# Optimization experiments

Measured on AMD Instinct MI355X. Metric: run time of the kernel, lower is better.

## Reference

```python
import jax, jax.numpy as jnp
import numpy as np

# Fixed hierarchical grouping of the 15 regions into 5 groups of 3 (from split_regions)
SPLIT_IDX = np.array([[0, 1, 8], [2, 4, 6], [3, 5, 7], [9, 11, 13], [10, 12, 14]])
BN_EPS = 1e-5


def _bn_relu(x, g, b):
    # BatchNorm over (batch, spatial) dims in training-stats mode, then ReLU
    mu = jnp.mean(x, axis=(0, 2, 3), keepdims=True)
    var = jnp.var(x, axis=(0, 2, 3), keepdims=True)
    xn = (x - mu) * jax.lax.rsqrt(var + BN_EPS)
    return jax.nn.relu(xn * g[None, :, None, None] + b[None, :, None, None])


def _local_agg(x, params):
    # x: [B, Cin, G, K]; pointwise conv (1x1) -> BN -> ReLU per layer, then max over K
    for W, g, b in params:
        x = jnp.einsum('oi,bigk->bogk', W, x)
        x = _bn_relu(x, g, b)
    return jnp.max(x, axis=-1)  # [B, Cout, G]


def setup_inputs() -> dict:
    key = jax.random.key(0)
    ks = jax.random.split(key, 8)
    B, G, K = 32, 15, 2048
    inp = {"local_regions": jax.random.normal(ks[0], (B, G, K, 3), jnp.float32)}
    chans = [(3, 64, 64), (67, 128, 128), (131, 256, 256)]
    ki = 1
    for li, (c0, c1, c2) in enumerate(chans):
        for wi, (co, ci) in enumerate([(c1, c0), (c2, c1)]):
            inp[f"la{li}_w{wi}"] = jax.random.normal(ks[ki], (co, ci), jnp.float32) * (1.0 / np.sqrt(ci))
            inp[f"la{li}_g{wi}"] = jnp.ones((co,), jnp.float32)
            inp[f"la{li}_b{wi}"] = jnp.zeros((co,), jnp.float32)
            ki += 1
    return inp


def reference(local_regions,
              la0_w0, la0_g0, la0_b0, la0_w1, la0_g1, la0_b1,
              la1_w0, la1_g0, la1_b0, la1_w1, la1_g1, la1_b1,
              la2_w0, la2_g0, la2_b0, la2_w1, la2_g1, la2_b1):
    la0 = [(la0_w0, la0_g0, la0_b0), (la0_w1, la0_g1, la0_b1)]
    la1 = [(la1_w0, la1_g0, la1_b0), (la1_w1, la1_g1, la1_b1)]
    la2 = [(la2_w0, la2_g0, la2_b0), (la2_w1, la2_g1, la2_b1)]
    idx = jnp.asarray(SPLIT_IDX)

    x = jnp.transpose(local_regions, (0, 3, 1, 2))  # [B, 3, 15, K]
    centroids_1 = jnp.mean(x, axis=-1)              # [B, 3, 15]
    relative_1 = x - centroids_1[..., None]
    lf1 = _local_agg(relative_1, la0)               # [B, 64, 15]
    local_features = jnp.concatenate([centroids_1, lf1], axis=1)  # [B, 67, 15]

    # level 2: regroup 15 regions into [5, 3]
    lf1_s = jnp.transpose(lf1, (0, 2, 1))[:, idx, :]         # [B, 5, 3, 64]
    lr2 = jnp.transpose(centroids_1, (0, 2, 1))[:, idx, :]   # [B, 5, 3, 3]
    c2 = jnp.mean(lr2, axis=2)                               # [B, 5, 3]
    rel2 = lr2 - c2[:, :, None, :]
    feats2 = jnp.concatenate([rel2, lf1_s], axis=-1)         # [B, 5, 3, 67]
    feats2 = jnp.transpose(feats2, (0, 3, 1, 2))             # [B, 67, 5, 3]
    lf2 = _local_agg(feats2, la1)                            # [B, 128, 5]

    # level 3: global
    c3 = jnp.mean(c2, axis=1)                                # [B, 3]
    rel3 = c2 - c3[:, None, :]                               # [B, 5, 3]
    lf2 = jnp.concatenate([jnp.transpose(rel3, (0, 2, 1)), lf2], axis=1)  # [B, 131, 5]
    lf2 = lf2[:, :, None, :]                                 # [B, 131, 1, 5]
    gf = _local_agg(lf2, la2)                                # [B, 256, 1]
    return gf.squeeze(2), local_features
```

## Files before the change

kernel.cpp:

```cpp
#include <hip/hip_runtime.h>
#include <math.h>

#define BB 32
#define GG 15
#define KK 2048
#define NB 480
#define N1F 983040.0f
#define EPS 1e-5f
#define PZN ((int)0xAAAAAAAA)

typedef _Float16 half8 __attribute__((ext_vector_type(8)));
typedef float f32x4 __attribute__((ext_vector_type(4)));

#define WS_CENT  0
#define WS_MN    1920
#define GSREL    63360
#define GBN1     63600
#define G2A      67440
#define G2B      67952
#define G3A      68464
#define G3B      69488
#define FSREL    70512
#define FBN1     70520
#define F2A      70648
#define F2B      70904
#define F3A      71160
#define F3B      71672
#define CNT_GRP  72184
#define CNT_SUP  72376
#define CNT_DONE 72382

#define SMEMF 7936

__device__ const int SIDX[15] = {0,1,8, 2,4,6, 3,5,7, 9,11,13, 10,12,14};

__device__ __forceinline__ float wave_sum(float v){
    for (int off = 32; off; off >>= 1) v += __shfl_down(v, off, 64);
    return v;
}
__device__ __forceinline__ float aloadf(const float* p){
    return __hip_atomic_load(p, __ATOMIC_RELAXED, __HIP_MEMORY_SCOPE_AGENT);
}
__device__ __forceinline__ int aloadi(const int* p){
    return __hip_atomic_load(p, __ATOMIC_RELAXED, __HIP_MEMORY_SCOPE_AGENT);
}
template<int SLP, class Fold>
__device__ __forceinline__ void gbar(int* wsi, int idx, int gi, int ngrp,
                                     int* sflag, Fold fold){
    __syncthreads();
    if (threadIdx.x == 0)
        sflag[0] = (atomicAdd(&wsi[CNT_GRP + idx*32 + gi], 1) == PZN + 15) ? 1 : 0;
    __syncthreads();
    if (sflag[0]) {
        if (threadIdx.x == 0)
            sflag[1] = (atomicAdd(&wsi[CNT_SUP + idx], 1) == PZN + ngrp - 1) ? 1 : 0;
        __syncthreads();
        if (sflag[1]) {
            fold();
            __syncthreads();
            if (threadIdx.x == 0) atomicExch(&wsi[CNT_DONE + idx], 1);
        }
    }
    if (threadIdx.x == 0) {
        int g = 0;
        while (aloadi(&wsi[CNT_DONE + idx]) != 1 && ++g < 4000000)
            __builtin_amdgcn_s_sleep(SLP);
    }
    __syncthreads();
    asm volatile("" ::: "memory");
}

__global__ void __launch_bounds__(256, 2) mega(
        const float* __restrict__ x,
        const float* __restrict__ w00, const float* __restrict__ g00, const float* __restrict__ b00,
        const float* __restrict__ w01, const float* __restrict__ g01, const float* __restrict__ b01,
        const float* __restrict__ w10, const float* __restrict__ g10, const float* __restrict__ b10,
        const float* __restrict__ w11, const float* __restrict__ g11, const float* __restrict__ b11,
        const float* __restrict__ w20, const float* __restrict__ g20, const float* __restrict__ b20,
        const float* __restrict__ w21, const float* __restrict__ g21, const float* __restrict__ b21,
        float* __restrict__ ws, float* __restrict__ out) {
    __shared__ __align__(16) float smemf[SMEMF];
    float* xls  = smemf;
    float* redM = smemf + 6144; float* redN = smemf + 6400;
    float* redS = smemf + 6656; float* redQ = smemf + 6912;
    float* bcast= smemf + 7168;
    int*   sflag= (int*)(smemf + 7916);
    float* s1ls  = smemf;
    float* t1ls  = smemf + 64;
    float* centls= smemf + 128;
    float* c2ls  = smemf + 176;
    float* c3ls  = smemf + 192;
    float* f2ls  = smemf + 256;
    float* vls   = smemf + 1280;
    float* f3ls  = smemf + 3200;
    float* u3ls  = smemf + 3968;
    int* wsi = (int*)ws;

    int bid = blockIdx.x, tid = threadIdx.x;
    int b_ = bid / GG, g_ = bid % GG;
    int wv = tid >> 6, lane = tid & 63, l15 = lane & 15, quad = lane >> 4;
    int gi = bid >> 4;

    {
        const float4* xp4 = (const float4*)(x + (size_t)bid * KK * 3);
        float4* xls4 = (float4*)xls;
        #pragma unroll
        for (int i = 0; i < 6; i++) xls4[i*256 + tid] = xp4[i*256 + tid];
        __syncthreads();
        float m[9] = {0,0,0,0,0,0,0,0,0};
        float a[24];
        const float* bp = &xls[tid*24];
        #pragma unroll
        for (int i = 0; i < 6; i++)
            *reinterpret_cast<float4*>(&a[i*4]) = *reinterpret_cast<const float4*>(&bp[i*4]);
        #pragma unroll
        for (int p = 0; p < 8; p++) {
            float ax=a[p*3], ay=a[p*3+1], az=a[p*3+2];
            m[0]+=ax; m[1]+=ay; m[2]+=az;
            m[3]=fmaf(ax,ax,m[3]); m[4]=fmaf(ay,ay,m[4]); m[5]=fmaf(az,az,m[5]);
            m[6]=fmaf(ax,ay,m[6]); m[7]=fmaf(ax,az,m[7]); m[8]=fmaf(ay,az,m[8]);
        }
        #pragma unroll
        for (int q = 0; q < 9; q++) {
            float v = wave_sum(m[q]);
            if (lane == 0) redM[q*4 + wv] = v;
        }
        __syncthreads();
        if (tid == 0) {
            float t[9];
            #pragma unroll
            for (int q = 0; q < 9; q++) t[q] = redM[q*4]+redM[q*4+1]+redM[q*4+2]+redM[q*4+3];
            float c0 = t[0]/KK, c1 = t[1]/KK, c2 = t[2]/KK;
            bcast[0]=c0; bcast[1]=c1; bcast[2]=c2;
            out[8192 + b_*(67*GG) + 0*GG + g_] = c0;
            out[8192 + b_*(67*GG) + 1*GG + g_] = c1;
            out[8192 + b_*(67*GG) + 2*GG + g_] = c2;
            atomicExch(&ws[WS_CENT + bid*4 + 0], c0);
            atomicExch(&ws[WS_CENT + bid*4 + 1], c1);
            atomicExch(&ws[WS_CENT + bid*4 + 2], c2);
            redM[40] = t[3] - KK*c0*c0;  redM[41] = t[4] - KK*c1*c1;
            redM[42] = t[5] - KK*c2*c2;  redM[43] = t[6] - KK*c0*c1;
            redM[44] = t[7] - KK*c0*c2;  redM[45] = t[8] - KK*c1*c2;
        }
        __syncthreads();
    }
    if (tid < 6) atomicAdd(&ws[GSREL + gi*8 + tid], redM[40 + tid]);

    half8 afA[4], afB[4];
    #pragma unroll
    for (int t = 0; t < 4; t++)
        #pragma unroll
        for (int j = 0; j < 8; j++) {
            afA[t][j] = (_Float16)w01[(t*16 + l15)*64 + quad*8 + j];
            afB[t][j] = (_Float16)w01[(t*16 + l15)*64 + 32 + quad*8 + j];
        }
    gbar<8>(wsi, 0, gi, 30, sflag, [&]{
        if (tid < 6) {
            float acc = 0.f;
            #pragma unroll
            for (int s = 0; s < 30; s++) acc += aloadf(&ws[GSREL + s*8 + tid]);
            atomicExch(&ws[FSREL + tid], acc);
        }
    });

    if (tid < 6) bcast[3+tid] = aloadf(&ws[FSREL + tid]) / N1F;
    __syncthreads();
    float c0 = bcast[0], c1 = bcast[1], c2v = bcast[2];
    float S00=bcast[3], S11=bcast[4], S22=bcast[5], S01=bcast[6], S02=bcast[7], S12=bcast[8];

    float wa0[8], wa1[8], wa2[8], ba[8], wb0[8], wb1[8], wb2[8], bb[8];
    #pragma unroll
    for (int j = 0; j < 8; j++) {
        int cA = quad*8 + j;
        float u0=w00[cA*3+0], u1=w00[cA*3+1], u2=w00[cA*3+2];
        float var = u0*u0*S00 + u1*u1*S11 + u2*u2*S22
                  + 2.f*(u0*u1*S01 + u0*u2*S02 + u1*u2*S12);
        float a1 = g00[cA]*rsqrtf(var + EPS);
        wa0[j]=a1*u0; wa1[j]=a1*u1; wa2[j]=a1*u2; ba[j]=b00[cA];
        int cB = cA + 32;
        float v0=w00[cB*3+0], v1=w00[cB*3+1], v2=w00[cB*3+2];
        float varB = v0*v0*S00 + v1*v1*S11 + v2*v2*S22
                   + 2.f*(v0*v1*S01 + v0*v2*S02 + v1*v2*S12);
        float a1B = g00[cB]*rsqrtf(varB + EPS);
        wb0[j]=a1B*v0; wb1[j]=a1B*v1; wb2[j]=a1B*v2; bb[j]=b00[cB];
    }
    float mx[16], mn[16], sm[16], sq[16];
    #pragma unroll
    for (int s = 0; s < 16; s++) { mx[s]=-1e30f; mn[s]=1e30f; sm[s]=0.f; sq[s]=0.f; }

    for (int it = 0; it < 32; it++) {
        int k = it*64 + wv*16 + l15;
        float r0 = xls[k*3+0]-c0, r1 = xls[k*3+1]-c1, r2 = xls[k*3+2]-c2v;
        half8 bf0, bf1;
        #pragma unroll
        for (int j = 0; j < 8; j++) {
            float pA = fmaf(wa0[j],r0, fmaf(wa1[j],r1, fmaf(wa2[j],r2, ba[j])));
            bf0[j] = (_Float16)fmaxf(pA, 0.f);
            float pB = fmaf(wb0[j],r0, fmaf(wb1[j],r1, fmaf(wb2[j],r2, bb[j])));
            bf1[j] = (_Float16)fmaxf(pB, 0.f);
        }
        #pragma unroll
        for (int t = 0; t < 4; t++) {
            f32x4 acc = {0.f,0.f,0.f,0.f};
            acc = __builtin_amdgcn_mfma_f32_16x16x32_f16(afA[t], bf0, acc, 0, 0, 0);
            acc = __builtin_amdgcn_mfma_f32_16x16x32_f16(afB[t], bf1, acc, 0, 0, 0);
            #pragma unroll
            for (int r = 0; r < 4; r++) {
                float h = acc[r];
                int s = t*4 + r;
                mx[s]=fmaxf(mx[s],h); mn[s]=fminf(mn[s],h);
                sm[s]+=h;             sq[s]=fmaf(h,h,sq[s]);
            }
        }
    }
    #pragma unroll
    for (int m = 1; m < 16; m <<= 1) {
        #pragma unroll
        for (int s = 0; s < 16; s++) {
            mx[s] = fmaxf(mx[s], __shfl_xor(mx[s], m, 64));
            mn[s] = fminf(mn[s], __shfl_xor(mn[s], m, 64));
            sm[s] += __shfl_xor(sm[s], m, 64);
            sq[s] += __shfl_xor(sq[s], m, 64);
        }
    }
    __syncthreads();
    if (l15 == 0) {
        #pragma unroll
        for (int t = 0; t < 4; t++)
            #pragma unroll
            for (int r = 0; r < 4; r++) {
                int o = t*16 + quad*4 + r;
                redM[wv*64+o]=mx[t*4+r]; redN[wv*64+o]=mn[t*4+r];
                redS[wv*64+o]=sm[t*4+r]; redQ[wv*64+o]=sq[t*4+r];
            }
    }
    __syncthreads();
    float Mreg = -1e30f, Nreg = 1e30f;
    if (tid < 64) {
        float S=0.f, Q=0.f;
        #pragma unroll
        for (int w = 0; w < 4; w++) {
            Mreg = fmaxf(Mreg, redM[w*64+tid]); Nreg = fminf(Nreg, redN[w*64+tid]);
            S += redS[w*64+tid];               Q += redQ[w*64+tid];
        }
        atomicAdd(&ws[GBN1 + gi*128 + tid], S);
        atomicAdd(&ws[GBN1 + gi*128 + 64 + tid], Q);
        atomicExch(&ws[WS_MN + bid*128 + tid], Mreg);
        atomicExch(&ws[WS_MN + bid*128 + 64 + tid], Nreg);
    }
    gbar<8>(wsi, 1, gi, 30, sflag, [&]{
        if (tid < 128) {
            float acc = 0.f;
            #pragma unroll
            for (int s = 0; s < 30; s++) acc += aloadf(&ws[GBN1 + s*128 + tid]);
            atomicExch(&ws[FBN1 + tid], acc);
        }
    });

    if (tid < 64) {
        float SM = aloadf(&ws[FBN1 + tid]);
        float SQ = aloadf(&ws[FBN1 + 64 + tid]);
        float mean = SM / N1F;
        float var  = SQ / N1F - mean*mean;
        float s1 = g01[tid]*rsqrtf(var + EPS);
        float t1 = b01[tid] - mean*s1;
        float val = fmaxf(fmaf(s1, (s1 >= 0.f) ? Mreg : Nreg, t1), 0.f);
        out[8192 + b_*(67*GG) + (3+tid)*GG + g_] = val;
        s1ls[tid] = s1; t1ls[tid] = t1;
    }
    if (g_ != 0) return;

    int git = b_ >> 4;
    if (tid < 45) centls[tid] = aloadf(&ws[WS_CENT + (b_*GG + tid/3)*4 + tid%3]);
    __syncthreads();
    if (tid < 15) {
        int s = tid/3, i = tid%3;
        c2ls[tid] = (centls[SIDX[s*3+0]*3+i] + centls[SIDX[s*3+1]*3+i]
                   + centls[SIDX[s*3+2]*3+i]) * (1.f/3.f);
    }
    __syncthreads();
    if (tid < 3)
        c3ls[tid] = (c2ls[tid]+c2ls[3+tid]+c2ls[6+tid]+c2ls[9+tid]+c2ls[12+tid]) * 0.2f;
    if (tid < 45) {
        int p = tid/3, i = tid%3;
        f2ls[p*68 + i] = centls[SIDX[p]*3+i] - c2ls[(p/3)*3 + i];
    }
    for (int u = tid; u < 960; u += 256) {
        int p = u >> 6, ch = u & 63, gsrc = SIDX[p];
        float Mv = aloadf(&ws[WS_MN + (b_*GG + gsrc)*128 + ch]);
        float Nv = aloadf(&ws[WS_MN + (b_*GG + gsrc)*128 + 64 + ch]);
        float s1 = s1ls[ch], t1 = t1ls[ch];
        f2ls[p*68 + 3 + ch] = fmaxf(fmaf(s1, (s1 >= 0.f) ? Mv : Nv, t1), 0.f);
    }
    __syncthreads();

    int half = tid >> 7, oc = tid & 127, pbase = half*8, npts = 8 - half;
    float acc[8];
    #pragma unroll
    for (int q = 0; q < 8; q++) acc[q] = 0.f;
    {
        const float* wr = w10 + oc*67;
        #pragma unroll 4
        for (int c = 0; c < 67; c++) {
            float wv_ = wr[c];
            #pragma unroll
            for (int q = 0; q < 8; q++)
                acc[q] = fmaf(wv_, f2ls[(pbase+q)*68 + c], acc[q]);
        }
        float S = 0.f, Q = 0.f;
        #pragma unroll
        for (int q = 0; q < 8; q++) if (q < npts) { S += acc[q]; Q = fmaf(acc[q],acc[q],Q); }
        redS[tid] = S; redQ[tid] = Q;
        __syncthreads();
        if (tid < 128) {
            atomicAdd(&ws[G2A + git*256 + tid],       redS[tid] + redS[tid+128]);
            atomicAdd(&ws[G2A + git*256 + 128 + tid], redQ[tid] + redQ[tid+128]);
        }
    }
    gbar<2>(wsi, 2, git, 2, sflag, [&]{
        float a = aloadf(&ws[G2A + tid]) + aloadf(&ws[G2A + 256 + tid]);
        atomicExch(&ws[F2A + tid], a);
    });

    {
        float mean = aloadf(&ws[F2A + oc]) / 480.f;
        float var  = aloadf(&ws[F2A + 128 + oc]) / 480.f - mean*mean;
        float s2 = g10[oc]*rsqrtf(var + EPS), t2 = b10[oc] - mean*s2;
        #pragma unroll
        for (int q = 0; q < 8; q++) {
            float v = fmaxf(fmaf(s2, acc[q], t2), 0.f);
            if (q < npts) vls[(pbase+q)*128 + oc] = v;
        }
    }
    __syncthreads();
    #pragma unroll
    for (int q = 0; q < 8; q++) acc[q] = 0.f;
    {
        const float* wr = w11 + oc*128;
        #pragma unroll 4
        for (int c = 0; c < 128; c++) {
            float wv_ = wr[c];
            #pragma unroll
            for (int q = 0; q < 8; q++)
                acc[q] = fmaf(wv_, vls[(pbase+q)*128 + c], acc[q]);
        }
        float S = 0.f, Q = 0.f;
        #pragma unroll
        for (int q = 0; q < 8; q++) if (q < npts) { S += acc[q]; Q = fmaf(acc[q],acc[q],Q); }
        redS[tid] = S; redQ[tid] = Q;
        __syncthreads();
        if (tid < 128) {
            atomicAdd(&ws[G2B + git*256 + tid],       redS[tid] + redS[tid+128]);
            atomicAdd(&ws[G2B + git*256 + 128 + tid], redQ[tid] + redQ[tid+128]);
        }
    }
    gbar<2>(wsi, 3, git, 2, sflag, [&]{
        float a = aloadf(&ws[G2B + tid]) + aloadf(&ws[G2B + 256 + tid]);
        atomicExch(&ws[F2B + tid], a);
    });

    {
        float mean = aloadf(&ws[F2B + oc]) / 480.f;
        float var  = aloadf(&ws[F2B + 128 + oc]) / 480.f - mean*mean;
        float s3 = g11[oc]*rsqrtf(var + EPS), t3 = b11[oc] - mean*s3;
        #pragma unroll
        for (int q = 0; q < 8; q++) {
            float v = fmaxf(fmaf(s3, acc[q], t3), 0.f);
            if (q < npts) vls[(pbase+q)*128 + oc] = v;
        }
    }
    __syncthreads();
    for (int u = tid; u < 640; u += 256) {
        int s = u >> 7, o2 = u & 127;
        float m = fmaxf(fmaxf(vls[(3*s)*128+o2], vls[(3*s+1)*128+o2]),
                        vls[(3*s+2)*128+o2]);
        f3ls[s*132 + 3 + o2] = m;
    }
    if (tid < 15) {
        int s = tid/3, i = tid%3;
        f3ls[s*132 + i] = c2ls[tid] - c3ls[i];
    }
    __syncthreads();

    float a3[5];
    #pragma unroll
    for (int s = 0; s < 5; s++) a3[s] = 0.f;
    {
        const float* wr = w20 + tid*131;
        #pragma unroll 4
        for (int c = 0; c < 131; c++) {
            float wv_ = wr[c];
            #pragma unroll
            for (int s = 0; s < 5; s++)
                a3[s] = fmaf(wv_, f3ls[s*132 + c], a3[s]);
        }
        float S = 0.f, Q = 0.f;
        #pragma unroll
        for (int s = 0; s < 5; s++) { S += a3[s]; Q = fmaf(a3[s],a3[s],Q); }
        atomicAdd(&ws[G3A + git*512 + tid], S);
        atomicAdd(&ws[G3A + git*512 + 256 + tid], Q);
    }
    gbar<2>(wsi, 4, git, 2, sflag, [&]{
        float a0 = aloadf(&ws[G3A + tid])       + aloadf(&ws[G3A + 512 + tid]);
        float a1 = aloadf(&ws[G3A + 256 + tid]) + aloadf(&ws[G3A + 512 + 256 + tid]);
        atomicExch(&ws[F3A + tid], a0);
        atomicExch(&ws[F3A + 256 + tid], a1);
    });

    {
        float mean = aloadf(&ws[F3A + tid]) / 160.f;
        float var  = aloadf(&ws[F3A + 256 + tid]) / 160.f - mean*mean;
        float s4 = g20[tid]*rsqrtf(var + EPS), t4 = b20[tid] - mean*s4;
        #pragma unroll
        for (int s = 0; s < 5; s++)
            u3ls[s*256 + tid] = fmaxf(fmaf(s4, a3[s], t4), 0.f);
    }
    __syncthreads();
    #pragma unroll
    for (int s = 0; s < 5; s++) a3[s] = 0.f;
    {
        const float* wr = w21 + tid*256;
        #pragma unroll 4
        for (int c = 0; c < 256; c++) {
            float wv_ = wr[c];
            #pragma unroll
            for (int s = 0; s < 5; s++)
                a3[s] = fmaf(wv_, u3ls[s*256 + c], a3[s]);
        }
        float S = 0.f, Q = 0.f;
        #pragma unroll
        for (int s = 0; s < 5; s++) { S += a3[s]; Q = fmaf(a3[s],a3[s],Q); }
        atomicAdd(&ws[G3B + git*512 + tid], S);
        atomicAdd(&ws[G3B + git*512 + 256 + tid], Q);
    }
    gbar<2>(wsi, 5, git, 2, sflag, [&]{
        float a0 = aloadf(&ws[G3B + tid])       + aloadf(&ws[G3B + 512 + tid]);
        float a1 = aloadf(&ws[G3B + 256 + tid]) + aloadf(&ws[G3B + 512 + 256 + tid]);
        atomicExch(&ws[F3B + tid], a0);
        atomicExch(&ws[F3B + 256 + tid], a1);
    });

    {
        float mean = aloadf(&ws[F3B + tid]) / 160.f;
        float var  = aloadf(&ws[F3B + 256 + tid]) / 160.f - mean*mean;
        float s5 = g21[tid]*rsqrtf(var + EPS), t5 = b21[tid] - mean*s5;
        float m = -1e30f;
        #pragma unroll
        for (int s = 0; s < 5; s++)
            m = fmaxf(m, fmaxf(fmaf(s5, a3[s], t5), 0.f));
        out[b_*256 + tid] = m;
    }
}

extern "C" void kernel_launch(void* const* d_in, const int* in_sizes, int n_in,
                              void* d_out, int out_size, void* d_ws, size_t ws_size,
                              hipStream_t stream) {
    (void)in_sizes; (void)n_in; (void)out_size; (void)ws_size;
    const float* x   = (const float*)d_in[0];
    const float* w00 = (const float*)d_in[1];
    const float* g00 = (const float*)d_in[2];
    const float* b00 = (const float*)d_in[3];
    const float* w01 = (const float*)d_in[4];
    const float* g01 = (const float*)d_in[5];
    const float* b01 = (const float*)d_in[6];
    const float* w10 = (const float*)d_in[7];
    const float* g10 = (const float*)d_in[8];
    const float* b10 = (const float*)d_in[9];
    const float* w11 = (const float*)d_in[10];
    const float* g11 = (const float*)d_in[11];
    const float* b11 = (const float*)d_in[12];
    const float* w20 = (const float*)d_in[13];
    const float* g20 = (const float*)d_in[14];
    const float* b20 = (const float*)d_in[15];
    const float* w21 = (const float*)d_in[16];
    const float* g21 = (const float*)d_in[17];
    const float* b21 = (const float*)d_in[18];
    float* out = (float*)d_out;
    float* ws  = (float*)d_ws;

    mega<<<NB, 256, 0, stream>>>(x, w00,g00,b00, w01,g01,b01, w10,g10,b10,
                                 w11,g11,b11, w20,g20,b20, w21,g21,b21, ws, out);
}
```

Before: 191.1 us.

## Replace hierarchical fold barriers with flat counter barriers and per-batch partial slots

Measured after the change: 203.8 us. +6.6%, slower.

```diff
diff --git a/kernel.cpp b/kernel.cpp
--- a/kernel.cpp
+++ b/kernel.cpp
@@ -1,7 +1,6 @@
 #include <hip/hip_runtime.h>
 #include <math.h>
 
-#define BB 32
 #define GG 15
 #define KK 2048
 #define NB 480
@@ -12,23 +11,22 @@
 typedef _Float16 half8 __attribute__((ext_vector_type(8)));
 typedef float f32x4 __attribute__((ext_vector_type(4)));
 
-#define WS_CENT  0
-#define WS_MN    1920
-#define GSREL    63360
-#define GBN1     63600
-#define G2A      67440
-#define G2B      67952
-#define G3A      68464
-#define G3B      69488
-#define FSREL    70512
-#define FBN1     70520
-#define F2A      70648
-#define F2B      70904
-#define F3A      71160
-#define F3B      71672
-#define CNT_GRP  72184
-#define CNT_SUP  72376
-#define CNT_DONE 72382
+#define CENT  0
+#define GSREL 1920
+#define GBN1  2160
+#define SELO  6256
+#define FBN1  36976
+#define P2A   37104
+#define P2B   45296
+#define P3A   53488
+#define P3B   69872
+#define CA0   86256
+#define CA1   86272
+#define CD1   86288
+#define CT2   86304
+#define CT3   86320
+#define CT4   86336
+#define CT5   86352
 
 #define SMEMF 7936
 
@@ -44,26 +42,13 @@
 __device__ __forceinline__ int aloadi(const int* p){
     return __hip_atomic_load(p, __ATOMIC_RELAXED, __HIP_MEMORY_SCOPE_AGENT);
 }
-template<int SLP, class Fold>
-__device__ __forceinline__ void gbar(int* wsi, int idx, int gi, int ngrp,
-                                     int* sflag, Fold fold){
-    __syncthreads();
-    if (threadIdx.x == 0)
-        sflag[0] = (atomicAdd(&wsi[CNT_GRP + idx*32 + gi], 1) == PZN + 15) ? 1 : 0;
-    __syncthreads();
-    if (sflag[0]) {
-        if (threadIdx.x == 0)
-            sflag[1] = (atomicAdd(&wsi[CNT_SUP + idx], 1) == PZN + ngrp - 1) ? 1 : 0;
-        __syncthreads();
-        if (sflag[1]) {
-            fold();
-            __syncthreads();
-            if (threadIdx.x == 0) atomicExch(&wsi[CNT_DONE + idx], 1);
-        }
-    }
+template<int SLP>
+__device__ __forceinline__ void fbar(int* c, int target){
+    __syncthreads();
     if (threadIdx.x == 0) {
+        atomicAdd(c, 1);
         int g = 0;
-        while (aloadi(&wsi[CNT_DONE + idx]) != 1 && ++g < 4000000)
+        while (aloadi(c) != target && ++g < 8000000)
             __builtin_amdgcn_s_sleep(SLP);
     }
     __syncthreads();
@@ -84,16 +69,17 @@
     float* redM = smemf + 6144; float* redN = smemf + 6400;
     float* redS = smemf + 6656; float* redQ = smemf + 6912;
     float* bcast= smemf + 7168;
-    int*   sflag= (int*)(smemf + 7916);
     float* s1ls  = smemf;
     float* t1ls  = smemf + 64;
-    float* centls= smemf + 128;
-    float* c2ls  = smemf + 176;
-    float* c3ls  = smemf + 192;
-    float* f2ls  = smemf + 256;
-    float* vls   = smemf + 1280;
-    float* f3ls  = smemf + 3200;
-    float* u3ls  = smemf + 3968;
+    float* centb = smemf + 128;
+    float* c2b   = smemf + 176;
+    float* c3b   = smemf + 192;
+    float* f2b   = smemf + 256;
+    float* vb    = smemf + 1344;
+    float* f3b   = smemf + 3392;
+    float* u3b   = smemf + 4052;
+    float* c2s   = smemf + 5332;
+    float* c2t   = smemf + 5460;
     int* wsi = (int*)ws;
 
     int bid = blockIdx.x, tid = threadIdx.x;
@@ -135,9 +121,9 @@
             out[8192 + b_*(67*GG) + 0*GG + g_] = c0;
             out[8192 + b_*(67*GG) + 1*GG + g_] = c1;
             out[8192 + b_*(67*GG) + 2*GG + g_] = c2;
-            atomicExch(&ws[WS_CENT + bid*4 + 0], c0);
-            atomicExch(&ws[WS_CENT + bid*4 + 1], c1);
-            atomicExch(&ws[WS_CENT + bid*4 + 2], c2);
+            atomicExch(&ws[CENT + bid*4 + 0], c0);
+            atomicExch(&ws[CENT + bid*4 + 1], c1);
+            atomicExch(&ws[CENT + bid*4 + 2], c2);
             redM[40] = t[3] - KK*c0*c0;  redM[41] = t[4] - KK*c1*c1;
             redM[42] = t[5] - KK*c2*c2;  redM[43] = t[6] - KK*c0*c1;
             redM[44] = t[7] - KK*c0*c2;  redM[45] = t[8] - KK*c1*c2;
@@ -154,16 +140,15 @@
             afA[t][j] = (_Float16)w01[(t*16 + l15)*64 + quad*8 + j];
             afB[t][j] = (_Float16)w01[(t*16 + l15)*64 + 32 + quad*8 + j];
         }
-    gbar<8>(wsi, 0, gi, 30, sflag, [&]{
-        if (tid < 6) {
-            float acc = 0.f;
-            #pragma unroll
-            for (int s = 0; s < 30; s++) acc += aloadf(&ws[GSREL + s*8 + tid]);
-            atomicExch(&ws[FSREL + tid], acc);
-        }
-    });
-
-    if (tid < 6) bcast[3+tid] = aloadf(&ws[FSREL + tid]) / N1F;
+
+    fbar<4>(&wsi[CA0], PZN + 480);
+
+    if (tid < 6) {
+        float acc = 0.f;
+        #pragma unroll
+        for (int s = 0; s < 30; s++) acc += aloadf(&ws[GSREL + s*8 + tid]);
+        bcast[3+tid] = acc / N1F;
+    }
     __syncthreads();
     float c0 = bcast[0], c1 = bcast[1], c2v = bcast[2];
     float S00=bcast[3], S11=bcast[4], S22=bcast[5], S01=bcast[6], S02=bcast[7], S12=bcast[8];
@@ -243,25 +228,43 @@
             Mreg = fmaxf(Mreg, redM[w*64+tid]); Nreg = fminf(Nreg, redN[w*64+tid]);
             S += redS[w*64+tid];               Q += redQ[w*64+tid];
         }
-        atomicAdd(&ws[GBN1 + gi*128 + tid], S);
-        atomicAdd(&ws[GBN1 + gi*128 + 64 + tid], Q);
-        atomicExch(&ws[WS_MN + bid*128 + tid], Mreg);
-        atomicExch(&ws[WS_MN + bid*128 + 64 + tid], Nreg);
-    }
-    gbar<8>(wsi, 1, gi, 30, sflag, [&]{
+        atomicAdd(&ws[GBN1 + b_*128 + tid], S);
+        atomicAdd(&ws[GBN1 + b_*128 + 64 + tid], Q);
+        float sel = (g01[tid] >= 0.f) ? Mreg : Nreg;
+        atomicExch(&ws[SELO + bid*64 + tid], sel);
+    }
+
+    __syncthreads();
+    if (tid == 0) atomicAdd(&wsi[CA1], 1);
+    if (bid == 0) {
+        if (tid == 0) {
+            int g = 0;
+            while (aloadi(&wsi[CA1]) != PZN + 480 && ++g < 8000000)
+                __builtin_amdgcn_s_sleep(2);
+        }
+        __syncthreads();
         if (tid < 128) {
             float acc = 0.f;
             #pragma unroll
-            for (int s = 0; s < 30; s++) acc += aloadf(&ws[GBN1 + s*128 + tid]);
+            for (int i = 0; i < 32; i++) acc += aloadf(&ws[GBN1 + i*128 + tid]);
             atomicExch(&ws[FBN1 + tid], acc);
         }
-    });
+        __syncthreads();
+        if (tid == 0) atomicAdd(&wsi[CD1], 1);
+    }
+    if (tid == 0) {
+        int g = 0;
+        while (aloadi(&wsi[CD1]) != PZN + 1 && ++g < 8000000)
+            __builtin_amdgcn_s_sleep(2);
+    }
+    __syncthreads();
+    asm volatile("" ::: "memory");
 
     if (tid < 64) {
-        float SM = aloadf(&ws[FBN1 + tid]);
-        float SQ = aloadf(&ws[FBN1 + 64 + tid]);
-        float mean = SM / N1F;
-        float var  = SQ / N1F - mean*mean;
+        float S = aloadf(&ws[FBN1 + tid]);
+        float Q = aloadf(&ws[FBN1 + 64 + tid]);
+        float mean = S / N1F;
+        float var  = Q / N1F - mean*mean;
         float s1 = g01[tid]*rsqrtf(var + EPS);
         float t1 = b01[tid] - mean*s1;
         float val = fmaxf(fmaf(s1, (s1 >= 0.f) ? Mreg : Nreg, t1), 0.f);
@@ -270,184 +273,208 @@
     }
     if (g_ != 0) return;
 
-    int git = b_ >> 4;
-    if (tid < 45) centls[tid] = aloadf(&ws[WS_CENT + (b_*GG + tid/3)*4 + tid%3]);
-    __syncthreads();
-    if (tid < 15) {
-        int s = tid/3, i = tid%3;
-        c2ls[tid] = (centls[SIDX[s*3+0]*3+i] + centls[SIDX[s*3+1]*3+i]
-                   + centls[SIDX[s*3+2]*3+i]) * (1.f/3.f);
-    }
-    __syncthreads();
-    if (tid < 3)
-        c3ls[tid] = (c2ls[tid]+c2ls[3+tid]+c2ls[6+tid]+c2ls[9+tid]+c2ls[12+tid]) * 0.2f;
-    if (tid < 45) {
-        int p = tid/3, i = tid%3;
-        f2ls[p*68 + i] = centls[SIDX[p]*3+i] - c2ls[(p/3)*3 + i];
-    }
-    for (int u = tid; u < 960; u += 256) {
-        int p = u >> 6, ch = u & 63, gsrc = SIDX[p];
-        float Mv = aloadf(&ws[WS_MN + (b_*GG + gsrc)*128 + ch]);
-        float Nv = aloadf(&ws[WS_MN + (b_*GG + gsrc)*128 + 64 + ch]);
-        float s1 = s1ls[ch], t1 = t1ls[ch];
-        f2ls[p*68 + 3 + ch] = fmaxf(fmaf(s1, (s1 >= 0.f) ? Mv : Nv, t1), 0.f);
-    }
-    __syncthreads();
-
-    int half = tid >> 7, oc = tid & 127, pbase = half*8, npts = 8 - half;
-    float acc[8];
-    #pragma unroll
-    for (int q = 0; q < 8; q++) acc[q] = 0.f;
+    int half_ = tid >> 7, oc = tid & 127, pbase = half_*8, npts = 8 - half_;
+    float acc1[8], acc2[8], a3[5], a3b[5];
+
     {
+        if (tid < 45) centb[tid] = aloadf(&ws[CENT + (b_*GG + tid/3)*4 + tid%3]);
+        if (tid >= 188) f2b[15*68 + (tid - 188)] = 0.f;
+        __syncthreads();
+        if (tid < 15) {
+            int s = tid/3, i = tid%3;
+            c2b[tid] = (centb[SIDX[s*3+0]*3+i] + centb[SIDX[s*3+1]*3+i]
+                      + centb[SIDX[s*3+2]*3+i]) * (1.f/3.f);
+        }
+        __syncthreads();
+        if (tid < 3)
+            c3b[tid] = (c2b[tid]+c2b[3+tid]+c2b[6+tid]+c2b[9+tid]+c2b[12+tid]) * 0.2f;
+        if (tid < 45) {
+            int p = tid/3, i = tid%3;
+            f2b[p*68 + i] = centb[SIDX[p]*3+i] - c2b[(p/3)*3 + i];
+        }
+        for (int u = tid; u < 960; u += 256) {
+            int p = u >> 6, ch = u & 63, src = b_*GG + SIDX[p];
+            float sel = aloadf(&ws[SELO + src*64 + ch]);
+            f2b[p*68 + 3 + ch] = fmaxf(fmaf(s1ls[ch], sel, t1ls[ch]), 0.f);
+        }
+        __syncthreads();
+        #pragma unroll
+        for (int q = 0; q < 8; q++) acc1[q] = 0.f;
         const float* wr = w10 + oc*67;
         #pragma unroll 4
         for (int c = 0; c < 67; c++) {
             float wv_ = wr[c];
             #pragma unroll
             for (int q = 0; q < 8; q++)
-                acc[q] = fmaf(wv_, f2ls[(pbase+q)*68 + c], acc[q]);
+                acc1[q] = fmaf(wv_, f2b[(pbase+q)*68 + c], acc1[q]);
         }
         float S = 0.f, Q = 0.f;
         #pragma unroll
-        for (int q = 0; q < 8; q++) if (q < npts) { S += acc[q]; Q = fmaf(acc[q],acc[q],Q); }
+        for (int q = 0; q < 8; q++) if (q < npts) { S += acc1[q]; Q = fmaf(acc1[q],acc1[q],Q); }
         redS[tid] = S; redQ[tid] = Q;
         __syncthreads();
         if (tid < 128) {
-            atomicAdd(&ws[G2A + git*256 + tid],       redS[tid] + redS[tid+128]);
-            atomicAdd(&ws[G2A + git*256 + 128 + tid], redQ[tid] + redQ[tid+128]);
-        }
-    }
-    gbar<2>(wsi, 2, git, 2, sflag, [&]{
-        float a = aloadf(&ws[G2A + tid]) + aloadf(&ws[G2A + 256 + tid]);
-        atomicExch(&ws[F2A + tid], a);
-    });
+            atomicExch(&ws[P2A + b_*256 + tid],       redS[tid] + redS[128 + tid]);
+            atomicExch(&ws[P2A + b_*256 + 128 + tid], redQ[tid] + redQ[128 + tid]);
+        }
+    }
+    fbar<1>(&wsi[CT2], PZN + 32);
 
     {
-        float mean = aloadf(&ws[F2A + oc]) / 480.f;
-        float var  = aloadf(&ws[F2A + 128 + oc]) / 480.f - mean*mean;
-        float s2 = g10[oc]*rsqrtf(var + EPS), t2 = b10[oc] - mean*s2;
-        #pragma unroll
-        for (int q = 0; q < 8; q++) {
-            float v = fmaxf(fmaf(s2, acc[q], t2), 0.f);
-            if (q < npts) vls[(pbase+q)*128 + oc] = v;
-        }
-    }
-    __syncthreads();
-    #pragma unroll
-    for (int q = 0; q < 8; q++) acc[q] = 0.f;
+        if (tid < 128) {
+            float S = 0.f, Q = 0.f;
+            #pragma unroll
+            for (int i = 0; i < 32; i++) {
+                S += aloadf(&ws[P2A + i*256 + tid]);
+                Q += aloadf(&ws[P2A + i*256 + 128 + tid]);
+            }
+            float mean = S / 480.f, var = Q / 480.f - mean*mean;
+            float s2 = g10[tid]*rsqrtf(var + EPS);
+            c2s[tid] = s2; c2t[tid] = b10[tid] - mean*s2;
+            vb[15*128 + tid] = 0.f;
+        }
+        __syncthreads();
+        {
+            float s2 = c2s[oc], t2 = c2t[oc];
+            #pragma unroll
+            for (int q = 0; q < 8; q++) {
+                float v = fmaxf(fmaf(s2, acc1[q], t2), 0.f);
+                if (q < npts) vb[(pbase+q)*128 + oc] = v;
+            }
+        }
+        __syncthreads();
+        #pragma unroll
+        for (int q = 0; q < 8; q++) acc2[q] = 0.f;
+        const float4* w4 = (const float4*)(w11 + oc*128);
+        #pragma unroll 2
+        for (int c4 = 0; c4 < 32; c4++) {
+            float4 wv4 = w4[c4];
+            int cb = c4*4;
+            #pragma unroll
+            for (int q = 0; q < 8; q++) {
+                const float* vrow = &vb[(pbase+q)*128];
+                acc2[q] = fmaf(wv4.x, vrow[cb+0], acc2[q]);
+                acc2[q] = fmaf(wv4.y, vrow[cb+1], acc2[q]);
+                acc2[q] = fmaf(wv4.z, vrow[cb+2], acc2[q]);
+                acc2[q] = fmaf(wv4.w, vrow[cb+3], acc2[q]);
+            }
+        }
+        float S = 0.f, Q = 0.f;
+        #pragma unroll
+        for (int q = 0; q < 8; q++) if (q < npts) { S += acc2[q]; Q = fmaf(acc2[q],acc2[q],Q); }
+        redS[tid] = S; redQ[tid] = Q;
+        __syncthreads();
+        if (tid < 128) {
+            atomicExch(&ws[P2B + b_*256 + tid],       redS[tid] + redS[128 + tid]);
+            atomicExch(&ws[P2B + b_*256 + 128 + tid], redQ[tid] + redQ[128 + tid]);
+        }
+    }
+    fbar<1>(&wsi[CT3], PZN + 32);
+
     {
-        const float* wr = w11 + oc*128;
-        #pragma unroll 4
-        for (int c = 0; c < 128; c++) {
-            float wv_ = wr[c];
-            #pragma unroll
-            for (int q = 0; q < 8; q++)
-                acc[q] = fmaf(wv_, vls[(pbase+q)*128 + c], acc[q]);
-        }
-        float S = 0.f, Q = 0.f;
-        #pragma unroll
-        for (int q = 0; q < 8; q++) if (q < npts) { S += acc[q]; Q = fmaf(acc[q],acc[q],Q); }
-        redS[tid] = S; redQ[tid] = Q;
-        __syncthreads();
         if (tid < 128) {
-            atomicAdd(&ws[G2B + git*256 + tid],       redS[tid] + redS[tid+128]);
-            atomicAdd(&ws[G2B + git*256 + 128 + tid], redQ[tid] + redQ[tid+128]);
-        }
-    }
-    gbar<2>(wsi, 3, git, 2, sflag, [&]{
-        float a = aloadf(&ws[G2B + tid]) + aloadf(&ws[G2B + 256 + tid]);
-        atomicExch(&ws[F2B + tid], a);
-    });
-
-    {
-        float mean = aloadf(&ws[F2B + oc]) / 480.f;
-        float var  = aloadf(&ws[F2B + 128 + oc]) / 480.f - mean*mean;
-        float s3 = g11[oc]*rsqrtf(var + EPS), t3 = b11[oc] - mean*s3;
-        #pragma unroll
-        for (int q = 0; q < 8; q++) {
-            float v = fmaxf(fmaf(s3, acc[q], t3), 0.f);
-            if (q < npts) vls[(pbase+q)*128 + oc] = v;
-        }
-    }
-    __syncthreads();
-    for (int u = tid; u < 640; u += 256) {
-        int s = u >> 7, o2 = u & 127;
-        float m = fmaxf(fmaxf(vls[(3*s)*128+o2], vls[(3*s+1)*128+o2]),
-                        vls[(3*s+2)*128+o2]);
-        f3ls[s*132 + 3 + o2] = m;
-    }
-    if (tid < 15) {
-        int s = tid/3, i = tid%3;
-        f3ls[s*132 + i] = c2ls[tid] - c3ls[i];
-    }
-    __syncthreads();
-
-    float a3[5];
-    #pragma unroll
-    for (int s = 0; s < 5; s++) a3[s] = 0.f;
-    {
+            float S = 0.f, Q = 0.f;
+            #pragma unroll
+            for (int i = 0; i < 32; i++) {
+                S += aloadf(&ws[P2B + i*256 + tid]);
+                Q += aloadf(&ws[P2B + i*256 + 128 + tid]);
+            }
+            float mean = S / 480.f, var = Q / 480.f - mean*mean;
+            float s3 = g11[tid]*rsqrtf(var + EPS);
+            c2s[tid] = s3; c2t[tid] = b11[tid] - mean*s3;
+        }
+        __syncthreads();
+        {
+            float s3 = c2s[oc], t3 = c2t[oc];
+            #pragma unroll
+            for (int q = 0; q < 8; q++) {
+                float v = fmaxf(fmaf(s3, acc2[q], t3), 0.f);
+                if (q < npts) vb[(pbase+q)*128 + oc] = v;
+            }
+        }
+        __syncthreads();
+        for (int u = tid; u < 640; u += 256) {
+            int s = u >> 7, ch = u & 127;
+            f3b[s*132 + 3 + ch] = fmaxf(fmaxf(vb[(3*s)*128+ch], vb[(3*s+1)*128+ch]),
+                                        vb[(3*s+2)*128+ch]);
+        }
+        if (tid < 15) {
+            int s = tid/3, i = tid%3;
+            f3b[s*132 + i] = c2b[tid] - c3b[i];
+        }
+        __syncthreads();
+        #pragma unroll
+        for (int s = 0; s < 5; s++) a3[s] = 0.f;
         const float* wr = w20 + tid*131;
         #pragma unroll 4
         for (int c = 0; c < 131; c++) {
             float wv_ = wr[c];
             #pragma unroll
             for (int s = 0; s < 5; s++)
-                a3[s] = fmaf(wv_, f3ls[s*132 + c], a3[s]);
+                a3[s] = fmaf(wv_, f3b[s*132 + c], a3[s]);
         }
         float S = 0.f, Q = 0.f;
         #pragma unroll
         for (int s = 0; s < 5; s++) { S += a3[s]; Q = fmaf(a3[s],a3[s],Q); }
-        atomicAdd(&ws[G3A + git*512 + tid], S);
-        atomicAdd(&ws[G3A + git*512 + 256 + tid], Q);
-    }
-    gbar<2>(wsi, 4, git, 2, sflag, [&]{
-        float a0 = aloadf(&ws[G3A + tid])       + aloadf(&ws[G3A + 512 + tid]);
-        float a1 = aloadf(&ws[G3A + 256 + tid]) + aloadf(&ws[G3A + 512 + 256 + tid]);
-        atomicExch(&ws[F3A + tid], a0);
-        atomicExch(&ws[F3A + 256 + tid], a1);
-    });
+        atomicExch(&ws[P3A + b_*512 + tid], S);
+        atomicExch(&ws[P3A + b_*512 + 256 + tid], Q);
+    }
+    fbar<1>(&wsi[CT4], PZN + 32);
 
     {
-        float mean = aloadf(&ws[F3A + tid]) / 160.f;
-        float var  = aloadf(&ws[F3A + 256 + tid]) / 160.f - mean*mean;
-        float s4 = g20[tid]*rsqrtf(var + EPS), t4 = b20[tid] - mean*s4;
+        {
+            float S = 0.f, Q = 0.f;
+            #pragma unroll
+            for (int i = 0; i < 32; i++) {
+                S += aloadf(&ws[P3A + i*512 + tid]);
+                Q += aloadf(&ws[P3A + i*512 + 256 + tid]);
+            }
+            float mean = S / 160.f, var = Q / 160.f - mean*mean;
+            float s4 = g20[tid]*rsqrtf(var + EPS);
+            float t4 = b20[tid] - mean*s4;
+            #pragma unroll
+            for (int s = 0; s < 5; s++)
+                u3b[s*256 + tid] = fmaxf(fmaf(s4, a3[s], t4), 0.f);
+        }
+        __syncthreads();
+        #pragma unroll
+        for (int s = 0; s < 5; s++) a3b[s] = 0.f;
+        const float4* w4 = (const float4*)(w21 + tid*256);
+        #pragma unroll 2
+        for (int c4 = 0; c4 < 64; c4++) {
+            float4 wv4 = w4[c4];
+            int cb = c4*4;
+            #pragma unroll
+            for (int s = 0; s < 5; s++) {
+                const float* ur = &u3b[s*256];
+                a3b[s] = fmaf(wv4.x, ur[cb+0], a3b[s]);
+                a3b[s] = fmaf(wv4.y, ur[cb+1], a3b[s]);
+                a3b[s] = fmaf(wv4.z, ur[cb+2], a3b[s]);
+                a3b[s] = fmaf(wv4.w, ur[cb+3], a3b[s]);
+            }
+        }
+        float S = 0.f, Q = 0.f;
+        #pragma unroll
+        for (int s = 0; s < 5; s++) { S += a3b[s]; Q = fmaf(a3b[s],a3b[s],Q); }
+        atomicExch(&ws[P3B + b_*512 + tid], S);
+        atomicExch(&ws[P3B + b_*512 + 256 + tid], Q);
+    }
+    fbar<1>(&wsi[CT5], PZN + 32);
+
+    {
+        float S = 0.f, Q = 0.f;
+        #pragma unroll
+        for (int i = 0; i < 32; i++) {
+            S += aloadf(&ws[P3B + i*512 + tid]);
+            Q += aloadf(&ws[P3B + i*512 + 256 + tid]);
+        }
+        float mean = S / 160.f, var = Q / 160.f - mean*mean;
+        float s5 = g21[tid]*rsqrtf(var + EPS);
+        float t5 = b21[tid] - mean*s5;
+        float m = -1e30f;
         #pragma unroll
         for (int s = 0; s < 5; s++)
-            u3ls[s*256 + tid] = fmaxf(fmaf(s4, a3[s], t4), 0.f);
-    }
-    __syncthreads();
-    #pragma unroll
-    for (int s = 0; s < 5; s++) a3[s] = 0.f;
-    {
-        const float* wr = w21 + tid*256;
-        #pragma unroll 4
-        for (int c = 0; c < 256; c++) {
-            float wv_ = wr[c];
-            #pragma unroll
-            for (int s = 0; s < 5; s++)
-                a3[s] = fmaf(wv_, u3ls[s*256 + c], a3[s]);
-        }
-        float S = 0.f, Q = 0.f;
-        #pragma unroll
-        for (int s = 0; s < 5; s++) { S += a3[s]; Q = fmaf(a3[s],a3[s],Q); }
-        atomicAdd(&ws[G3B + git*512 + tid], S);
-        atomicAdd(&ws[G3B + git*512 + 256 + tid], Q);
-    }
-    gbar<2>(wsi, 5, git, 2, sflag, [&]{
-        float a0 = aloadf(&ws[G3B + tid])       + aloadf(&ws[G3B + 512 + tid]);
-        float a1 = aloadf(&ws[G3B + 256 + tid]) + aloadf(&ws[G3B + 512 + 256 + tid]);
-        atomicExch(&ws[F3B + tid], a0);
-        atomicExch(&ws[F3B + 256 + tid], a1);
-    });
-
-    {
-        float mean = aloadf(&ws[F3B + tid]) / 160.f;
-        float var  = aloadf(&ws[F3B + 256 + tid]) / 160.f - mean*mean;
-        float s5 = g21[tid]*rsqrtf(var + EPS), t5 = b21[tid] - mean*s5;
-        float m = -1e30f;
-        #pragma unroll
-        for (int s = 0; s < 5; s++)
-            m = fmaxf(m, fmaxf(fmaf(s5, a3[s], t5), 0.f));
+            m = fmaxf(m, fmaxf(fmaf(s5, a3b[s], t5), 0.f));
         out[b_*256 + tid] = m;
     }
 }
```
